# Kernel tuning notes

Measured on AMD Instinct MI355X. Metric: run time of the kernel, lower is better.

## Reference

```python
import jax, jax.numpy as jnp
import numpy as np

B, S, F, OWN, H, E = 16384, 37, 17, 9, 256, 128
NOUT = 7 + 16


def setup_inputs() -> dict:
    key = jax.random.key(0)
    ks = jax.random.split(key, 22)
    obs = jax.random.normal(ks[0], (B, S + 1, F), dtype=jnp.float32)
    pad = jax.random.bernoulli(ks[1], 0.3, (B, S))
    obs = obs.at[:, 1:, :].multiply(jnp.where(pad, 0.0, 1.0)[:, :, None])

    def init(k, shape):
        return jax.random.normal(k, shape, dtype=jnp.float32) * 0.05

    params = dict(
        sW1=init(ks[2], (F, H)), sb1=jnp.zeros((H,), jnp.float32),
        sW2=init(ks[3], (H, H)), sb2=jnp.zeros((H,), jnp.float32),
        sW3=init(ks[4], (H, E)), sb3=jnp.zeros((E,), jnp.float32),
        aW1=init(ks[5], (E + OWN, H)), ab1=jnp.zeros((H,), jnp.float32),
        aW2=init(ks[6], (H, H)), ab2=jnp.zeros((H,), jnp.float32),
        aW3=init(ks[7], (H, NOUT)), ab3=jnp.zeros((NOUT,), jnp.float32),
        vW1=init(ks[8], (E + OWN, H)), vb1=jnp.zeros((H,), jnp.float32),
        vW2=init(ks[9], (H, H)), vb2=jnp.zeros((H,), jnp.float32),
        vW3=init(ks[10], (H, 1)), vb3=jnp.zeros((1,), jnp.float32),
    )
    return {"obs": obs, **params}


def reference(obs, sW1, sb1, sW2, sb2, sW3, sb3,
              aW1, ab1, aW2, ab2, aW3, ab3,
              vW1, vb1, vW2, vb2, vW3, vb3):
    s_own = obs[:, 0, :OWN]                      # [B, 9]
    seqs = obs[:, 1:, :]                         # [B, 37, 17]
    # non-padded mask: rows whose abs-sum is nonzero
    mask = (jnp.sum(jnp.abs(seqs), axis=-1) != 0).astype(obs.dtype)  # [B, 37]

    # shared MLP applied to every row; masked positions zeroed before the
    # pooling sum (equivalent to gather->MLP->scatter into zeros->sum)
    h = jax.nn.relu(seqs @ sW1 + sb1)
    h = jax.nn.relu(h @ sW2 + sb2)
    h = jax.nn.relu(h @ sW3 + sb3)               # [B, 37, E]
    h = h * mask[..., None]
    summed = jnp.sum(h, axis=1)                  # [B, E]

    cat = jnp.concatenate([summed, s_own], axis=1)  # [B, E+9]

    a = jax.nn.relu(cat @ aW1 + ab1)
    a = jax.nn.relu(a @ aW2 + ab2)
    action_logits = a @ aW3 + ab3                # [B, 23]

    v = jax.nn.relu(cat @ vW1 + vb1)
    v = jax.nn.relu(v @ vW2 + vb2)
    value = (v @ vW3 + vb3).reshape(-1)          # [B]

    return action_logits, value
```

## Files before the change

kernel.cpp:

```cpp
#include <hip/hip_runtime.h>
#include <hip/hip_bf16.h>

#define B_    16384
#define S_    37
#define F_    17
#define OWN_  9
#define NOUT_ 23
#define OBS_ROW 646

typedef __bf16 bf16x8 __attribute__((ext_vector_type(8)));
typedef __bf16 bf16x4 __attribute__((ext_vector_type(4)));
typedef float  f32x4  __attribute__((ext_vector_type(4)));

#define MFMA(a,b,c) __builtin_amdgcn_mfma_f32_16x16x32_bf16(a, b, c, 0, 0, 0)

#define W1F_OFF   0
#define W2F_OFF   8192
#define W3F_OFF   73728
#define AW1F_OFF  106496
#define AW2F_OFF  147456
#define AW3F_OFF  212992
#define VW1F_OFF  221184
#define VW2F_OFF  262144
#define VW3F_OFF  327680
#define PREP_TOTAL8 41472

__global__ void prep_kernel(const float* __restrict__ sW1, const float* __restrict__ sW2,
                            const float* __restrict__ sW3, const float* __restrict__ aW1,
                            const float* __restrict__ aW2, const float* __restrict__ aW3,
                            const float* __restrict__ vW1, const float* __restrict__ vW2,
                            const float* __restrict__ vW3, __bf16* __restrict__ ws)
{
    int j8 = blockIdx.x * 256 + threadIdx.x;
    const float* src; __bf16* dst; int Np, Ks, Ns;
    if (j8 < 1024)                { dst = ws + W1F_OFF;  src = sW1; Np = 256; Ks = 17;  Ns = 256; }
    else if ((j8 -= 1024) < 8192) { dst = ws + W2F_OFF;  src = sW2; Np = 256; Ks = 256; Ns = 256; }
    else if ((j8 -= 8192) < 4096) { dst = ws + W3F_OFF;  src = sW3; Np = 128; Ks = 256; Ns = 128; }
    else if ((j8 -= 4096) < 5120) { dst = ws + AW1F_OFF; src = aW1; Np = 256; Ks = 137; Ns = 256; }
    else if ((j8 -= 5120) < 8192) { dst = ws + AW2F_OFF; src = aW2; Np = 256; Ks = 256; Ns = 256; }
    else if ((j8 -= 8192) < 1024) { dst = ws + AW3F_OFF; src = aW3; Np = 32;  Ks = 256; Ns = 23;  }
    else if ((j8 -= 1024) < 5120) { dst = ws + VW1F_OFF; src = vW1; Np = 256; Ks = 137; Ns = 256; }
    else if ((j8 -= 5120) < 8192) { dst = ws + VW2F_OFF; src = vW2; Np = 256; Ks = 256; Ns = 256; }
    else { j8 -= 8192;              dst = ws + VW3F_OFF; src = vW3; Np = 16;  Ks = 256; Ns = 1;   }
    const int c = j8 / Np, n = j8 - c * Np;
    bf16x8 pk;
    #pragma unroll
    for (int e = 0; e < 8; ++e) {
        const int k = c * 8 + e;
        const float v = (k < Ks && n < Ns) ? src[k * Ns + n] : 0.f;
        pk[e] = (__bf16)v;
    }
    *(bf16x8*)(dst + (size_t)j8 * 8) = pk;
}

__global__ __launch_bounds__(512) __attribute__((amdgpu_waves_per_eu(2, 2)))
void fused_kernel(
    const float* __restrict__ obs,
    const float* __restrict__ sb1, const float* __restrict__ sb2, const float* __restrict__ sb3,
    const float* __restrict__ ab1, const float* __restrict__ ab2, const float* __restrict__ ab3,
    const float* __restrict__ vb1, const float* __restrict__ vb2, const float* __restrict__ vb3,
    const __bf16* __restrict__ ws, float* __restrict__ out)
{
    __shared__ __align__(16) char pool[148480];
    __bf16* act1 = (__bf16*)pool;
    __bf16* act2 = (__bf16*)(pool + 65536);
    __bf16* xs0  = (__bf16*)(pool + 131072);
    __bf16* xs1  = (__bf16*)(pool + 139264);
    float*  sm0  = (float*)(pool + 147456);
    float*  sm1  = (float*)(pool + 147968);
    __bf16* catf = (__bf16*)(pool + 131072);
    float*  partial = (float*)pool;

    const __bf16* W1f  = ws + W1F_OFF;
    const __bf16* W2f  = ws + W2F_OFF;
    const __bf16* W3f  = ws + W3F_OFF;
    const __bf16* AW1f = ws + AW1F_OFF;
    const __bf16* AW2f = ws + AW2F_OFF;
    const __bf16* AW3f = ws + AW3F_OFF;
    const __bf16* VW1f = ws + VW1F_OFF;
    const __bf16* VW2f = ws + VW2F_OFF;
    const __bf16* VW3f = ws + VW3F_OFF;

    const int tid  = threadIdx.x;
    const int wave = tid >> 6;
    const int lane = tid & 63;
    const int q    = lane >> 4;
    const int l16  = lane & 15;
    const int qh   = q >> 1;
    const int e4   = (q & 1) * 4;
    const int b0   = blockIdx.x * 16;
    const int nc   = wave & 3;
    const int mr   = wave >> 2;
    const f32x4 z4 = {0.f, 0.f, 0.f, 0.f};

    const int sr  = tid >> 2;
    const int sp  = tid & 3;
    const int sb  = sr & 15;
    const int ssl = sr >> 4;
    const int nf  = (sp == 3) ? 5 : 4;
    const float* obs_row = obs + (size_t)(b0 + sb) * OBS_ROW;

    #pragma unroll
    for (int i = 0; i < 2; ++i)
        ((f32x4*)xs0)[tid + i * 512] = z4;

    bf16x8 w1f[2], w2f[8][2], w3f[2][8];
    f32x4 b1q[2], b2q[2], b3q[2];
    #pragma unroll
    for (int nt = 0; nt < 2; ++nt) {
        const int n = wave * 32 + nt * 16 + l16;
        w1f[nt] = *(const bf16x8*)(W1f + ((size_t)q * 256 + n) * 8);
        b1q[nt] = *(const f32x4*)(sb1 + wave * 32 + nt * 16 + q * 4);
        b2q[nt] = *(const f32x4*)(sb2 + wave * 32 + nt * 16 + q * 4);
        b3q[nt] = *(const f32x4*)(sb3 + nc * 32 + nt * 16 + q * 4);
        #pragma unroll
        for (int k = 0; k < 8; ++k) {
            w2f[k][nt] = *(const bf16x8*)(W2f + ((size_t)(k * 4 + q) * 256 + n) * 8);
            w3f[nt][k] = *(const bf16x8*)(W3f + ((size_t)(k * 4 + q) * 128 + nc * 32 + nt * 16 + l16) * 8);
        }
    }

    __syncthreads();

    {
        const float* p = obs_row + (ssl + 1) * F_ + sp * 4;
        float psum = 0.f;
        #pragma unroll
        for (int f = 0; f < 5; ++f) {
            if (f < nf) {
                const float v = p[f];
                psum += fabsf(v);
                const int c = sp * 4 + f;
                xs0[((c >> 3) * 128 + sr) * 8 + (c & 7)] = (__bf16)v;
            }
        }
        psum += __shfl_xor(psum, 1);
        psum += __shfl_xor(psum, 2);
        if (sp == 0) sm0[sr] = psum;
    }
    __syncthreads();

    f32x4 vsum[2] = {z4, z4};

    for (int it = 0; it < 5; ++it) {
        __bf16* xc  = (it & 1) ? xs1 : xs0;
        __bf16* xn  = (it & 1) ? xs0 : xs1;
        float*  smc = (it & 1) ? sm1 : sm0;
        float*  smn = (it & 1) ? sm0 : sm1;

        const int s_nx = (it + 1) * 8 + ssl;
        const bool st_valid = (it < 4) && (s_nx < S_);
        float stv[5];
        if (st_valid) {
            const float* p = obs_row + (s_nx + 1) * F_ + sp * 4;
            #pragma unroll
            for (int f = 0; f < 5; ++f)
                if (f < nf) stv[f] = p[f];
        }

        #pragma unroll 2
        for (int m = 0; m < 8; ++m) {
            const bf16x8 xm = *(const bf16x8*)(xc + (q * 128 + m * 16 + l16) * 8);
            #pragma unroll
            for (int nt = 0; nt < 2; ++nt) {
                const f32x4 h = MFMA(w1f[nt], xm, b1q[nt]);
                float v0 = h[0] > 0.f ? h[0] : 0.f;
                float v1 = h[1] > 0.f ? h[1] : 0.f;
                float v2 = h[2] > 0.f ? h[2] : 0.f;
                float v3 = h[3] > 0.f ? h[3] : 0.f;
                const bf16x4 pk = {(__bf16)v0, (__bf16)v1, (__bf16)v2, (__bf16)v3};
                *(bf16x4*)(act1 + ((wave * 4 + nt * 2 + qh) * 128 + m * 16 + l16) * 8 + e4) = pk;
            }
        }
        __syncthreads();

        if (it < 4) {
            float psum = 0.f;
            if (st_valid) {
                #pragma unroll
                for (int f = 0; f < 5; ++f) {
                    if (f < nf) {
                        const float v = stv[f];
                        psum += fabsf(v);
                        const int c = sp * 4 + f;
                        xn[((c >> 3) * 128 + sr) * 8 + (c & 7)] = (__bf16)v;
                    }
                }
            }
            psum += __shfl_xor(psum, 1);
            psum += __shfl_xor(psum, 2);
            if (sp == 0) smn[sr] = st_valid ? psum : 0.f;
        }

        #pragma unroll 1
        for (int mq = 0; mq < 4; ++mq) {
            f32x4 h2[2][2];
            #pragma unroll
            for (int nt = 0; nt < 2; ++nt)
                #pragma unroll
                for (int m = 0; m < 2; ++m) h2[nt][m] = b2q[nt];
            #pragma unroll
            for (int k = 0; k < 8; ++k) {
                const int k8 = k * 4 + q;
                #pragma unroll
                for (int m = 0; m < 2; ++m) {
                    const bf16x8 a = *(const bf16x8*)(act1 + (k8 * 128 + mq * 32 + m * 16 + l16) * 8);
                    h2[0][m] = MFMA(w2f[k][0], a, h2[0][m]);
                    h2[1][m] = MFMA(w2f[k][1], a, h2[1][m]);
                }
            }
            #pragma unroll
            for (int nt = 0; nt < 2; ++nt)
                #pragma unroll
                for (int m = 0; m < 2; ++m) {
                    float v0 = h2[nt][m][0] > 0.f ? h2[nt][m][0] : 0.f;
                    float v1 = h2[nt][m][1] > 0.f ? h2[nt][m][1] : 0.f;
                    float v2 = h2[nt][m][2] > 0.f ? h2[nt][m][2] : 0.f;
                    float v3 = h2[nt][m][3] > 0.f ? h2[nt][m][3] : 0.f;
                    const bf16x4 pk = {(__bf16)v0, (__bf16)v1, (__bf16)v2, (__bf16)v3};
                    *(bf16x4*)(act2 + ((wave * 4 + nt * 2 + qh) * 128 + mq * 32 + m * 16 + l16) * 8 + e4) = pk;
                }
        }
        __syncthreads();

        #pragma unroll 1
        for (int mi = 0; mi < 4; ++mi) {
            f32x4 h3[2] = {b3q[0], b3q[1]};
            #pragma unroll
            for (int k = 0; k < 8; ++k) {
                const int k8 = k * 4 + q;
                const bf16x8 a = *(const bf16x8*)(act2 + (k8 * 128 + mr * 64 + mi * 16 + l16) * 8);
                h3[0] = MFMA(w3f[0][k], a, h3[0]);
                h3[1] = MFMA(w3f[1][k], a, h3[1]);
            }
            const float mv = smc[mr * 64 + mi * 16 + l16];
            #pragma unroll
            for (int nt = 0; nt < 2; ++nt)
                #pragma unroll
                for (int r = 0; r < 4; ++r) {
                    float v = h3[nt][r];
                    v = v > 0.f ? v : 0.f;
                    vsum[nt][r] += (mv != 0.f) ? v : 0.f;
                }
        }
    }

    if (mr == 0) {
        #pragma unroll
        for (int nt = 0; nt < 2; ++nt)
            #pragma unroll
            for (int r = 0; r < 4; ++r)
                partial[(nc * 32 + nt * 16 + q * 4 + r) * 16 + l16] = vsum[nt][r];
    }
    if (tid < 16) {
        const float* p = obs + (size_t)(b0 + tid) * OBS_ROW;
        #pragma unroll
        for (int c = 0; c < 8; ++c) catf[(16 * 16 + tid) * 8 + c] = (__bf16)p[c];
        catf[(17 * 16 + tid) * 8 + 0] = (__bf16)p[8];
        #pragma unroll
        for (int c = 1; c < 8; ++c) catf[(17 * 16 + tid) * 8 + c] = (__bf16)0.f;
    } else if (tid < 32) {
        const int rr = tid - 16;
        #pragma unroll
        for (int c = 0; c < 8; ++c) {
            catf[(18 * 16 + rr) * 8 + c] = (__bf16)0.f;
            catf[(19 * 16 + rr) * 8 + c] = (__bf16)0.f;
        }
    }
    __syncthreads();

    if (mr == 1) {
        #pragma unroll
        for (int nt = 0; nt < 2; ++nt) {
            f32x4 t = vsum[nt];
            #pragma unroll
            for (int r = 0; r < 4; ++r)
                t[r] += partial[(nc * 32 + nt * 16 + q * 4 + r) * 16 + l16];
            const bf16x4 pk = {(__bf16)t[0], (__bf16)t[1], (__bf16)t[2], (__bf16)t[3]};
            *(bf16x4*)(catf + ((nc * 4 + nt * 2 + qh) * 16 + l16) * 8 + e4) = pk;
        }
    }
    __syncthreads();

    {
        f32x4 ha[2], hv[2];
        #pragma unroll
        for (int nt = 0; nt < 2; ++nt) {
            ha[nt] = *(const f32x4*)(ab1 + wave * 32 + nt * 16 + q * 4);
            hv[nt] = *(const f32x4*)(vb1 + wave * 32 + nt * 16 + q * 4);
        }
        #pragma unroll
        for (int k = 0; k < 5; ++k) {
            const int k8 = k * 4 + q;
            const bf16x8 ca = *(const bf16x8*)(catf + (k8 * 16 + l16) * 8);
            #pragma unroll
            for (int nt = 0; nt < 2; ++nt) {
                const int n = wave * 32 + nt * 16 + l16;
                const bf16x8 ba = *(const bf16x8*)(AW1f + ((size_t)k8 * 256 + n) * 8);
                const bf16x8 bv = *(const bf16x8*)(VW1f + ((size_t)k8 * 256 + n) * 8);
                ha[nt] = MFMA(ba, ca, ha[nt]);
                hv[nt] = MFMA(bv, ca, hv[nt]);
            }
        }
        #pragma unroll
        for (int nt = 0; nt < 2; ++nt) {
            float a0 = ha[nt][0] > 0.f ? ha[nt][0] : 0.f;
            float a1 = ha[nt][1] > 0.f ? ha[nt][1] : 0.f;
            float a2 = ha[nt][2] > 0.f ? ha[nt][2] : 0.f;
            float a3 = ha[nt][3] > 0.f ? ha[nt][3] : 0.f;
            float u0 = hv[nt][0] > 0.f ? hv[nt][0] : 0.f;
            float u1 = hv[nt][1] > 0.f ? hv[nt][1] : 0.f;
            float u2 = hv[nt][2] > 0.f ? hv[nt][2] : 0.f;
            float u3 = hv[nt][3] > 0.f ? hv[nt][3] : 0.f;
            const bf16x4 pa = {(__bf16)a0, (__bf16)a1, (__bf16)a2, (__bf16)a3};
            const bf16x4 pv = {(__bf16)u0, (__bf16)u1, (__bf16)u2, (__bf16)u3};
            const int c = wave * 4 + nt * 2 + qh;
            *(bf16x4*)(act1 + (c * 128 + l16) * 8 + e4)      = pa;
            *(bf16x4*)(act1 + (c * 128 + 16 + l16) * 8 + e4) = pv;
        }
    }
    __syncthreads();

    {
        f32x4 ha[2], hv[2];
        #pragma unroll
        for (int nt = 0; nt < 2; ++nt) {
            ha[nt] = *(const f32x4*)(ab2 + wave * 32 + nt * 16 + q * 4);
            hv[nt] = *(const f32x4*)(vb2 + wave * 32 + nt * 16 + q * 4);
        }
        #pragma unroll
        for (int k = 0; k < 8; ++k) {
            const int k8 = k * 4 + q;
            const bf16x8 a0 = *(const bf16x8*)(act1 + (k8 * 128 + l16) * 8);
            const bf16x8 a1 = *(const bf16x8*)(act1 + (k8 * 128 + 16 + l16) * 8);
            #pragma unroll
            for (int nt = 0; nt < 2; ++nt) {
                const int n = wave * 32 + nt * 16 + l16;
                const bf16x8 ba = *(const bf16x8*)(AW2f + ((size_t)k8 * 256 + n) * 8);
                const bf16x8 bv = *(const bf16x8*)(VW2f + ((size_t)k8 * 256 + n) * 8);
                ha[nt] = MFMA(ba, a0, ha[nt]);
                hv[nt] = MFMA(bv, a1, hv[nt]);
            }
        }
        #pragma unroll
        for (int nt = 0; nt < 2; ++nt) {
            float a0 = ha[nt][0] > 0.f ? ha[nt][0] : 0.f;
            float a1 = ha[nt][1] > 0.f ? ha[nt][1] : 0.f;
            float a2 = ha[nt][2] > 0.f ? ha[nt][2] : 0.f;
            float a3 = ha[nt][3] > 0.f ? ha[nt][3] : 0.f;
            float u0 = hv[nt][0] > 0.f ? hv[nt][0] : 0.f;
            float u1 = hv[nt][1] > 0.f ? hv[nt][1] : 0.f;
            float u2 = hv[nt][2] > 0.f ? hv[nt][2] : 0.f;
            float u3 = hv[nt][3] > 0.f ? hv[nt][3] : 0.f;
            const bf16x4 pa = {(__bf16)a0, (__bf16)a1, (__bf16)a2, (__bf16)a3};
            const bf16x4 pv = {(__bf16)u0, (__bf16)u1, (__bf16)u2, (__bf16)u3};
            const int c = wave * 4 + nt * 2 + qh;
            *(bf16x4*)(act2 + (c * 128 + l16) * 8 + e4)      = pa;
            *(bf16x4*)(act2 + (c * 128 + 16 + l16) * 8 + e4) = pv;
        }
    }
    __syncthreads();

    if (wave < 2) {
        f32x4 acc = z4;
        #pragma unroll
        for (int k = 0; k < 8; ++k) {
            const int k8 = k * 4 + q;
            const bf16x8 a0 = *(const bf16x8*)(act2 + (k8 * 128 + l16) * 8);
            const bf16x8 bf = *(const bf16x8*)(AW3f + ((size_t)k8 * 32 + wave * 16 + l16) * 8);
            acc = MFMA(bf, a0, acc);
        }
        const int nb = wave * 16 + q * 4;
        #pragma unroll
        for (int r = 0; r < 4; ++r) {
            const int n = nb + r;
            if (n < NOUT_)
                out[(size_t)(b0 + l16) * NOUT_ + n] = acc[r] + ab3[n];
        }
    } else if (wave == 2) {
        f32x4 acc = z4;
        #pragma unroll
        for (int k = 0; k < 8; ++k) {
            const int k8 = k * 4 + q;
            const bf16x8 a1 = *(const bf16x8*)(act2 + (k8 * 128 + 16 + l16) * 8);
            const bf16x8 bf = *(const bf16x8*)(VW3f + ((size_t)k8 * 16 + l16) * 8);
            acc = MFMA(bf, a1, acc);
        }
        if (q == 0)
            out[(size_t)B_ * NOUT_ + b0 + l16] = acc[0] + vb3[0];
    }
}

extern "C" void kernel_launch(void* const* d_in, const int* in_sizes, int n_in,
                              void* d_out, int out_size, void* d_ws, size_t ws_size,
                              hipStream_t stream)
{
    const float* obs = (const float*)d_in[0];
    const float* sW1 = (const float*)d_in[1];
    const float* sb1 = (const float*)d_in[2];
    const float* sW2 = (const float*)d_in[3];
    const float* sb2 = (const float*)d_in[4];
    const float* sW3 = (const float*)d_in[5];
    const float* sb3 = (const float*)d_in[6];
    const float* aW1 = (const float*)d_in[7];
    const float* ab1 = (const float*)d_in[8];
    const float* aW2 = (const float*)d_in[9];
    const float* ab2 = (const float*)d_in[10];
    const float* aW3 = (const float*)d_in[11];
    const float* ab3 = (const float*)d_in[12];
    const float* vW1 = (const float*)d_in[13];
    const float* vb1 = (const float*)d_in[14];
    const float* vW2 = (const float*)d_in[15];
    const float* vb2 = (const float*)d_in[16];
    const float* vW3 = (const float*)d_in[17];
    const float* vb3 = (const float*)d_in[18];

    __bf16* ws = (__bf16*)d_ws;
    float* out = (float*)d_out;

    hipLaunchKernelGGL(prep_kernel, dim3(PREP_TOTAL8 / 256), dim3(256), 0, stream,
                       sW1, sW2, sW3, aW1, aW2, aW3, vW1, vW2, vW3, ws);
    hipLaunchKernelGGL(fused_kernel, dim3(B_ / 16), dim3(512), 0, stream,
                       obs, sb1, sb2, sb3, ab1, ab2, ab3, vb1, vb2, vb3,
                       (const __bf16*)ws, out);
}
```

Before: 261.1 us.

## Double block to 1024 threads, splitting row halves and actor/critic heads across waves

```diff
diff --git a/kernel.cpp b/kernel.cpp
--- a/kernel.cpp
+++ b/kernel.cpp
@@ -53,7 +53,7 @@
     *(bf16x8*)(dst + (size_t)j8 * 8) = pk;
 }
 
-__global__ __launch_bounds__(512) __attribute__((amdgpu_waves_per_eu(2, 2)))
+__global__ __launch_bounds__(1024)
 void fused_kernel(
     const float* __restrict__ obs,
     const float* __restrict__ sb1, const float* __restrict__ sb2, const float* __restrict__ sb3,
@@ -89,29 +89,30 @@
     const int qh   = q >> 1;
     const int e4   = (q & 1) * 4;
     const int b0   = blockIdx.x * 16;
+    const int nw   = wave & 7;
+    const int rh   = wave >> 3;
     const int nc   = wave & 3;
-    const int mr   = wave >> 2;
+    const int mr4  = wave >> 2;
     const f32x4 z4 = {0.f, 0.f, 0.f, 0.f};
 
-    const int sr  = tid >> 2;
-    const int sp  = tid & 3;
+    const int sr  = tid >> 3;
+    const int sp  = tid & 7;
     const int sb  = sr & 15;
     const int ssl = sr >> 4;
-    const int nf  = (sp == 3) ? 5 : 4;
+    const int nf  = (sp == 7) ? 3 : 2;
     const float* obs_row = obs + (size_t)(b0 + sb) * OBS_ROW;
 
-    #pragma unroll
-    for (int i = 0; i < 2; ++i)
-        ((f32x4*)xs0)[tid + i * 512] = z4;
+    for (int i = tid; i < 1024; i += 1024)
+        ((f32x4*)xs0)[i] = z4;
 
     bf16x8 w1f[2], w2f[8][2], w3f[2][8];
     f32x4 b1q[2], b2q[2], b3q[2];
     #pragma unroll
     for (int nt = 0; nt < 2; ++nt) {
-        const int n = wave * 32 + nt * 16 + l16;
+        const int n = nw * 32 + nt * 16 + l16;
         w1f[nt] = *(const bf16x8*)(W1f + ((size_t)q * 256 + n) * 8);
-        b1q[nt] = *(const f32x4*)(sb1 + wave * 32 + nt * 16 + q * 4);
-        b2q[nt] = *(const f32x4*)(sb2 + wave * 32 + nt * 16 + q * 4);
+        b1q[nt] = *(const f32x4*)(sb1 + nw * 32 + nt * 16 + q * 4);
+        b2q[nt] = *(const f32x4*)(sb2 + nw * 32 + nt * 16 + q * 4);
         b3q[nt] = *(const f32x4*)(sb3 + nc * 32 + nt * 16 + q * 4);
         #pragma unroll
         for (int k = 0; k < 8; ++k) {
@@ -123,19 +124,20 @@
     __syncthreads();
 
     {
-        const float* p = obs_row + (ssl + 1) * F_ + sp * 4;
+        const float* p = obs_row + (ssl + 1) * F_ + sp * 2;
         float psum = 0.f;
         #pragma unroll
-        for (int f = 0; f < 5; ++f) {
+        for (int f = 0; f < 3; ++f) {
             if (f < nf) {
                 const float v = p[f];
                 psum += fabsf(v);
-                const int c = sp * 4 + f;
+                const int c = sp * 2 + f;
                 xs0[((c >> 3) * 128 + sr) * 8 + (c & 7)] = (__bf16)v;
             }
         }
         psum += __shfl_xor(psum, 1);
         psum += __shfl_xor(psum, 2);
+        psum += __shfl_xor(psum, 4);
         if (sp == 0) sm0[sr] = psum;
     }
     __syncthreads();
@@ -150,17 +152,17 @@
 
         const int s_nx = (it + 1) * 8 + ssl;
         const bool st_valid = (it < 4) && (s_nx < S_);
-        float stv[5];
+        float stv[3];
         if (st_valid) {
-            const float* p = obs_row + (s_nx + 1) * F_ + sp * 4;
-            #pragma unroll
-            for (int f = 0; f < 5; ++f)
+            const float* p = obs_row + (s_nx + 1) * F_ + sp * 2;
+            #pragma unroll
+            for (int f = 0; f < 3; ++f)
                 if (f < nf) stv[f] = p[f];
         }
 
         #pragma unroll 2
-        for (int m = 0; m < 8; ++m) {
-            const bf16x8 xm = *(const bf16x8*)(xc + (q * 128 + m * 16 + l16) * 8);
+        for (int m = 0; m < 4; ++m) {
+            const bf16x8 xm = *(const bf16x8*)(xc + (q * 128 + rh * 64 + m * 16 + l16) * 8);
             #pragma unroll
             for (int nt = 0; nt < 2; ++nt) {
                 const f32x4 h = MFMA(w1f[nt], xm, b1q[nt]);
@@ -169,7 +171,7 @@
                 float v2 = h[2] > 0.f ? h[2] : 0.f;
                 float v3 = h[3] > 0.f ? h[3] : 0.f;
                 const bf16x4 pk = {(__bf16)v0, (__bf16)v1, (__bf16)v2, (__bf16)v3};
-                *(bf16x4*)(act1 + ((wave * 4 + nt * 2 + qh) * 128 + m * 16 + l16) * 8 + e4) = pk;
+                *(bf16x4*)(act1 + ((nw * 4 + nt * 2 + qh) * 128 + rh * 64 + m * 16 + l16) * 8 + e4) = pk;
             }
         }
         __syncthreads();
@@ -178,22 +180,23 @@
             float psum = 0.f;
             if (st_valid) {
                 #pragma unroll
-                for (int f = 0; f < 5; ++f) {
+                for (int f = 0; f < 3; ++f) {
                     if (f < nf) {
                         const float v = stv[f];
                         psum += fabsf(v);
-                        const int c = sp * 4 + f;
+                        const int c = sp * 2 + f;
                         xn[((c >> 3) * 128 + sr) * 8 + (c & 7)] = (__bf16)v;
                     }
                 }
             }
             psum += __shfl_xor(psum, 1);
             psum += __shfl_xor(psum, 2);
+            psum += __shfl_xor(psum, 4);
             if (sp == 0) smn[sr] = st_valid ? psum : 0.f;
         }
 
         #pragma unroll 1
-        for (int mq = 0; mq < 4; ++mq) {
+        for (int mq = 0; mq < 2; ++mq) {
             f32x4 h2[2][2];
             #pragma unroll
             for (int nt = 0; nt < 2; ++nt)
@@ -204,7 +207,7 @@
                 const int k8 = k * 4 + q;
                 #pragma unroll
                 for (int m = 0; m < 2; ++m) {
-                    const bf16x8 a = *(const bf16x8*)(act1 + (k8 * 128 + mq * 32 + m * 16 + l16) * 8);
+                    const bf16x8 a = *(const bf16x8*)(act1 + (k8 * 128 + rh * 64 + mq * 32 + m * 16 + l16) * 8);
                     h2[0][m] = MFMA(w2f[k][0], a, h2[0][m]);
                     h2[1][m] = MFMA(w2f[k][1], a, h2[1][m]);
                 }
@@ -218,22 +221,22 @@
                     float v2 = h2[nt][m][2] > 0.f ? h2[nt][m][2] : 0.f;
                     float v3 = h2[nt][m][3] > 0.f ? h2[nt][m][3] : 0.f;
                     const bf16x4 pk = {(__bf16)v0, (__bf16)v1, (__bf16)v2, (__bf16)v3};
-                    *(bf16x4*)(act2 + ((wave * 4 + nt * 2 + qh) * 128 + mq * 32 + m * 16 + l16) * 8 + e4) = pk;
+                    *(bf16x4*)(act2 + ((nw * 4 + nt * 2 + qh) * 128 + rh * 64 + mq * 32 + m * 16 + l16) * 8 + e4) = pk;
                 }
         }
         __syncthreads();
 
         #pragma unroll 1
-        for (int mi = 0; mi < 4; ++mi) {
+        for (int mi = 0; mi < 2; ++mi) {
             f32x4 h3[2] = {b3q[0], b3q[1]};
             #pragma unroll
             for (int k = 0; k < 8; ++k) {
                 const int k8 = k * 4 + q;
-                const bf16x8 a = *(const bf16x8*)(act2 + (k8 * 128 + mr * 64 + mi * 16 + l16) * 8);
+                const bf16x8 a = *(const bf16x8*)(act2 + (k8 * 128 + mr4 * 32 + mi * 16 + l16) * 8);
                 h3[0] = MFMA(w3f[0][k], a, h3[0]);
                 h3[1] = MFMA(w3f[1][k], a, h3[1]);
             }
-            const float mv = smc[mr * 64 + mi * 16 + l16];
+            const float mv = smc[mr4 * 32 + mi * 16 + l16];
             #pragma unroll
             for (int nt = 0; nt < 2; ++nt)
                 #pragma unroll
@@ -245,12 +248,12 @@
         }
     }
 
-    if (mr == 0) {
+    if (mr4 != 0) {
         #pragma unroll
         for (int nt = 0; nt < 2; ++nt)
             #pragma unroll
             for (int r = 0; r < 4; ++r)
-                partial[(nc * 32 + nt * 16 + q * 4 + r) * 16 + l16] = vsum[nt][r];
+                partial[(mr4 - 1) * 2048 + (nc * 32 + nt * 16 + q * 4 + r) * 16 + l16] = vsum[nt][r];
     }
     if (tid < 16) {
         const float* p = obs + (size_t)(b0 + tid) * OBS_ROW;
@@ -269,13 +272,15 @@
     }
     __syncthreads();
 
-    if (mr == 1) {
+    if (mr4 == 0) {
         #pragma unroll
         for (int nt = 0; nt < 2; ++nt) {
             f32x4 t = vsum[nt];
             #pragma unroll
-            for (int r = 0; r < 4; ++r)
-                t[r] += partial[(nc * 32 + nt * 16 + q * 4 + r) * 16 + l16];
+            for (int r = 0; r < 4; ++r) {
+                const int idx = (nc * 32 + nt * 16 + q * 4 + r) * 16 + l16;
+                t[r] += partial[idx] + partial[2048 + idx] + partial[4096 + idx];
+            }
             const bf16x4 pk = {(__bf16)t[0], (__bf16)t[1], (__bf16)t[2], (__bf16)t[3]};
             *(bf16x4*)(catf + ((nc * 4 + nt * 2 + qh) * 16 + l16) * 8 + e4) = pk;
         }
@@ -283,80 +288,69 @@
     __syncthreads();
 
     {
-        f32x4 ha[2], hv[2];
-        #pragma unroll
-        for (int nt = 0; nt < 2; ++nt) {
-            ha[nt] = *(const f32x4*)(ab1 + wave * 32 + nt * 16 + q * 4);
-            hv[nt] = *(const f32x4*)(vb1 + wave * 32 + nt * 16 + q * 4);
-        }
+        const bool is_a = wave < 8;
+        const int  hw   = wave & 7;
+        const __bf16* HW1 = is_a ? AW1f : VW1f;
+        const float*  hb1 = is_a ? ab1  : vb1;
+        const int rowoff = is_a ? 0 : 16;
+        f32x4 hh[2];
+        #pragma unroll
+        for (int nt = 0; nt < 2; ++nt)
+            hh[nt] = *(const f32x4*)(hb1 + hw * 32 + nt * 16 + q * 4);
         #pragma unroll
         for (int k = 0; k < 5; ++k) {
             const int k8 = k * 4 + q;
             const bf16x8 ca = *(const bf16x8*)(catf + (k8 * 16 + l16) * 8);
             #pragma unroll
             for (int nt = 0; nt < 2; ++nt) {
-                const int n = wave * 32 + nt * 16 + l16;
-                const bf16x8 ba = *(const bf16x8*)(AW1f + ((size_t)k8 * 256 + n) * 8);
-                const bf16x8 bv = *(const bf16x8*)(VW1f + ((size_t)k8 * 256 + n) * 8);
-                ha[nt] = MFMA(ba, ca, ha[nt]);
-                hv[nt] = MFMA(bv, ca, hv[nt]);
+                const int n = hw * 32 + nt * 16 + l16;
+                const bf16x8 bw = *(const bf16x8*)(HW1 + ((size_t)k8 * 256 + n) * 8);
+                hh[nt] = MFMA(bw, ca, hh[nt]);
             }
         }
         #pragma unroll
         for (int nt = 0; nt < 2; ++nt) {
-            float a0 = ha[nt][0] > 0.f ? ha[nt][0] : 0.f;
-            float a1 = ha[nt][1] > 0.f ? ha[nt][1] : 0.f;
-            float a2 = ha[nt][2] > 0.f ? ha[nt][2] : 0.f;
-            float a3 = ha[nt][3] > 0.f ? ha[nt][3] : 0.f;
-            float u0 = hv[nt][0] > 0.f ? hv[nt][0] : 0.f;
-            float u1 = hv[nt][1] > 0.f ? hv[nt][1] : 0.f;
-            float u2 = hv[nt][2] > 0.f ? hv[nt][2] : 0.f;
-            float u3 = hv[nt][3] > 0.f ? hv[nt][3] : 0.f;
-            const bf16x4 pa = {(__bf16)a0, (__bf16)a1, (__bf16)a2, (__bf16)a3};
-            const bf16x4 pv = {(__bf16)u0, (__bf16)u1, (__bf16)u2, (__bf16)u3};
-            const int c = wave * 4 + nt * 2 + qh;
-            *(bf16x4*)(act1 + (c * 128 + l16) * 8 + e4)      = pa;
-            *(bf16x4*)(act1 + (c * 128 + 16 + l16) * 8 + e4) = pv;
+            float a0 = hh[nt][0] > 0.f ? hh[nt][0] : 0.f;
+            float a1 = hh[nt][1] > 0.f ? hh[nt][1] : 0.f;
+            float a2 = hh[nt][2] > 0.f ? hh[nt][2] : 0.f;
+            float a3 = hh[nt][3] > 0.f ? hh[nt][3] : 0.f;
+            const bf16x4 pk = {(__bf16)a0, (__bf16)a1, (__bf16)a2, (__bf16)a3};
+            const int c = hw * 4 + nt * 2 + qh;
+            *(bf16x4*)(act1 + (c * 128 + rowoff + l16) * 8 + e4) = pk;
         }
     }
     __syncthreads();
 
     {
-        f32x4 ha[2], hv[2];
-        #pragma unroll
-        for (int nt = 0; nt < 2; ++nt) {
-            ha[nt] = *(const f32x4*)(ab2 + wave * 32 + nt * 16 + q * 4);
-            hv[nt] = *(const f32x4*)(vb2 + wave * 32 + nt * 16 + q * 4);
-        }
+        const bool is_a = wave < 8;
+        const int  hw   = wave & 7;
+        const __bf16* HW2 = is_a ? AW2f : VW2f;
+        const float*  hb2 = is_a ? ab2  : vb2;
+        const int rowoff = is_a ? 0 : 16;
+        f32x4 hh[2];
+        #pragma unroll
+        for (int nt = 0; nt < 2; ++nt)
+            hh[nt] = *(const f32x4*)(hb2 + hw * 32 + nt * 16 + q * 4);
         #pragma unroll
         for (int k = 0; k < 8; ++k) {
             const int k8 = k * 4 + q;
-            const bf16x8 a0 = *(const bf16x8*)(act1 + (k8 * 128 + l16) * 8);
-            const bf16x8 a1 = *(const bf16x8*)(act1 + (k8 * 128 + 16 + l16) * 8);
+            const bf16x8 a0 = *(const bf16x8*)(act1 + (k8 * 128 + rowoff + l16) * 8);
             #pragma unroll
             for (int nt = 0; nt < 2; ++nt) {
-                const int n = wave * 32 + nt * 16 + l16;
-                const bf16x8 ba = *(const bf16x8*)(AW2f + ((size_t)k8 * 256 + n) * 8);
-                const bf16x8 bv = *(const bf16x8*)(VW2f + ((size_t)k8 * 256 + n) * 8);
-                ha[nt] = MFMA(ba, a0, ha[nt]);
-                hv[nt] = MFMA(bv, a1, hv[nt]);
+                const int n = hw * 32 + nt * 16 + l16;
+                const bf16x8 bw = *(const bf16x8*)(HW2 + ((size_t)k8 * 256 + n) * 8);
+                hh[nt] = MFMA(bw, a0, hh[nt]);
             }
         }
         #pragma unroll
         for (int nt = 0; nt < 2; ++nt) {
-            float a0 = ha[nt][0] > 0.f ? ha[nt][0] : 0.f;
-            float a1 = ha[nt][1] > 0.f ? ha[nt][1] : 0.f;
-            float a2 = ha[nt][2] > 0.f ? ha[nt][2] : 0.f;
-            float a3 = ha[nt][3] > 0.f ? ha[nt][3] : 0.f;
-            float u0 = hv[nt][0] > 0.f ? hv[nt][0] : 0.f;
-            float u1 = hv[nt][1] > 0.f ? hv[nt][1] : 0.f;
-            float u2 = hv[nt][2] > 0.f ? hv[nt][2] : 0.f;
-            float u3 = hv[nt][3] > 0.f ? hv[nt][3] : 0.f;
-            const bf16x4 pa = {(__bf16)a0, (__bf16)a1, (__bf16)a2, (__bf16)a3};
-            const bf16x4 pv = {(__bf16)u0, (__bf16)u1, (__bf16)u2, (__bf16)u3};
-            const int c = wave * 4 + nt * 2 + qh;
-            *(bf16x4*)(act2 + (c * 128 + l16) * 8 + e4)      = pa;
-            *(bf16x4*)(act2 + (c * 128 + 16 + l16) * 8 + e4) = pv;
+            float a0 = hh[nt][0] > 0.f ? hh[nt][0] : 0.f;
+            float a1 = hh[nt][1] > 0.f ? hh[nt][1] : 0.f;
+            float a2 = hh[nt][2] > 0.f ? hh[nt][2] : 0.f;
+            float a3 = hh[nt][3] > 0.f ? hh[nt][3] : 0.f;
+            const bf16x4 pk = {(__bf16)a0, (__bf16)a1, (__bf16)a2, (__bf16)a3};
+            const int c = hw * 4 + nt * 2 + qh;
+            *(bf16x4*)(act2 + (c * 128 + rowoff + l16) * 8 + e4) = pk;
         }
     }
     __syncthreads();
@@ -420,7 +414,7 @@
 
     hipLaunchKernelGGL(prep_kernel, dim3(PREP_TOTAL8 / 256), dim3(256), 0, stream,
                        sW1, sW2, sW3, aW1, aW2, aW3, vW1, vW2, vW3, ws);
-    hipLaunchKernelGGL(fused_kernel, dim3(B_ / 16), dim3(512), 0, stream,
+    hipLaunchKernelGGL(fused_kernel, dim3(B_ / 16), dim3(1024), 0, stream,
                        obs, sb1, sb2, sb3, ab1, ab2, ab3, vb1, vb2, vb3,
                        (const __bf16*)ws, out);
 }
```

Measured after the change: 863.6 us. +230.8%, slower.
